# Optimization experiments

Hardware: AMD Instinct MI355X
Metric: run time of the kernel (lower is better)

Reference implementation:

```python
import jax, jax.numpy as jnp
import numpy as np

N_NODES = 50000
N_EDGES = 800000
D_IN = 96
D_HID = 256
D_OUT = 2
N_GRAPHS = 64


def _gin_conv(x, src, dst, W1, b1, W2, b2):
    # GINConv with eps=0: MLP(x + sum_{j in N(i)} x_j)
    agg = jax.ops.segment_sum(x[src], dst, num_segments=x.shape[0])
    h = x + agg
    h = jax.nn.relu(h @ W1 + b1)
    return h @ W2 + b2


def setup_inputs() -> dict:
    key = jax.random.key(0)
    ks = jax.random.split(key, 12)
    x = jax.random.normal(ks[0], (N_NODES, D_IN), dtype=jnp.float32)
    edge_index = jax.random.randint(ks[1], (2, N_EDGES), 0, N_NODES, dtype=jnp.int64)
    batch = jnp.sort(jax.random.randint(ks[2], (N_NODES,), 0, N_GRAPHS, dtype=jnp.int64))

    def lin(k, fan_in, shape):
        bound = 1.0 / np.sqrt(fan_in)
        return jax.random.uniform(k, shape, jnp.float32, -bound, bound)

    W1 = lin(ks[3], D_IN, (D_IN, D_HID)); b1 = lin(ks[4], D_IN, (D_HID,))
    W2 = lin(ks[5], D_HID, (D_HID, D_HID)); b2 = lin(ks[6], D_HID, (D_HID,))
    V1 = lin(ks[7], D_HID, (D_HID, D_HID)); c1 = lin(ks[8], D_HID, (D_HID,))
    V2 = lin(ks[9], D_HID, (D_HID, D_HID)); c2 = lin(ks[10], D_HID, (D_HID,))
    Wl = lin(ks[11], D_HID, (D_HID, D_OUT)); bl = jnp.zeros((D_OUT,), jnp.float32)
    return {"x": x, "edge_index": edge_index, "batch": batch,
            "W1": W1, "b1": b1, "W2": W2, "b2": b2,
            "V1": V1, "c1": c1, "V2": V2, "c2": c2,
            "Wl": Wl, "bl": bl}


def reference(x, edge_index, batch, W1, b1, W2, b2, V1, c1, V2, c2, Wl, bl):
    src, dst = edge_index[0], edge_index[1]
    h = jax.nn.relu(_gin_conv(x, src, dst, W1, b1, W2, b2))
    h = _gin_conv(h, src, dst, V1, c1, V2, c2)
    # global_mean_pool over batch ids
    sums = jax.ops.segment_sum(h, batch, num_segments=N_GRAPHS)
    counts = jax.ops.segment_sum(jnp.ones((h.shape[0], 1), h.dtype), batch,
                                 num_segments=N_GRAPHS)
    pooled = sums / jnp.maximum(counts, 1.0)
    # dropout p=0.1 is identity in eval mode
    return pooled @ Wl + bl
```

## Files before the change

kernel.cpp:

```cpp
#include <hip/hip_runtime.h>

#define N_NODES 50000
#define N_EDGES 800000
#define D_IN 96
#define D_HID 256
#define N_GRAPHS 64

#define SCAN_NB ((N_NODES + 255) / 256)

typedef __attribute__((ext_vector_type(8))) short bf16x8;
typedef __attribute__((ext_vector_type(4))) float f32x4;

__device__ __forceinline__ unsigned short f2bf(float f) {
    union { float f; unsigned int u; } v; v.f = f;
    unsigned int r = (v.u + 0x7FFFu + ((v.u >> 16) & 1u)) >> 16;
    return (unsigned short)r;
}
__device__ __forceinline__ float bfLo(unsigned int u) {
    union { unsigned int u; float f; } v; v.u = u << 16; return v.f;
}
__device__ __forceinline__ float bfHi(unsigned int u) {
    union { unsigned int u; float f; } v; v.u = u & 0xFFFF0000u; return v.f;
}
__device__ __forceinline__ unsigned int packbf(float a, float b) {
    return (unsigned int)f2bf(a) | ((unsigned int)f2bf(b) << 16);
}

__global__ void k_count(const int* __restrict__ dst, int* __restrict__ deg, int E) {
    int e = blockIdx.x * blockDim.x + threadIdx.x;
    if (e < E) atomicAdd(&deg[dst[e]], 1);
}

__global__ __launch_bounds__(256) void k_scan1(const int* __restrict__ deg,
                                               int* __restrict__ bsum, int n) {
    __shared__ int red[256];
    int tid = threadIdx.x;
    int i = blockIdx.x * 256 + tid;
    red[tid] = (i < n) ? deg[i] : 0;
    __syncthreads();
    for (int off = 128; off > 0; off >>= 1) {
        if (tid < off) red[tid] += red[tid + off];
        __syncthreads();
    }
    if (tid == 0) bsum[blockIdx.x] = red[0];
}

__global__ __launch_bounds__(256) void k_scan2(int* __restrict__ bsum, int nb) {
    __shared__ int s[256];
    int tid = threadIdx.x;
    int v = (tid < nb) ? bsum[tid] : 0;
    s[tid] = v;
    __syncthreads();
    for (int off = 1; off < 256; off <<= 1) {
        int t = (tid >= off) ? s[tid - off] : 0;
        __syncthreads();
        s[tid] += t;
        __syncthreads();
    }
    if (tid < nb) bsum[tid] = s[tid] - v;
}

__global__ __launch_bounds__(256) void k_scan3(const int* __restrict__ deg,
                                               const int* __restrict__ bsum,
                                               int* __restrict__ rp,
                                               int* __restrict__ wp, int n) {
    __shared__ int s[256];
    int tid = threadIdx.x;
    int i = blockIdx.x * 256 + tid;
    int v = (i < n) ? deg[i] : 0;
    s[tid] = v;
    __syncthreads();
    for (int off = 1; off < 256; off <<= 1) {
        int t = (tid >= off) ? s[tid - off] : 0;
        __syncthreads();
        s[tid] += t;
        __syncthreads();
    }
    if (i < n) {
        int excl = s[tid] - v + bsum[blockIdx.x];
        rp[i] = excl;
        wp[i] = excl;
    }
    if (blockIdx.x == 0 && tid == 0) rp[n] = N_EDGES;
}

__global__ void k_scatter(const int* __restrict__ src, const int* __restrict__ dst,
                          int* __restrict__ wp, int* __restrict__ csr, int E) {
    int e = blockIdx.x * blockDim.x + threadIdx.x;
    if (e < E) {
        int p = atomicAdd(&wp[dst[e]], 1);
        csr[p] = src[e];
    }
}

__global__ __launch_bounds__(256) void k_x2bf(const float* __restrict__ x,
                                              unsigned short* __restrict__ xb, int n4) {
    int i = blockIdx.x * 256 + threadIdx.x;
    if (i >= n4) return;
    float4 v = ((const float4*)x)[i];
    ((uint2*)xb)[i] = make_uint2(packbf(v.x, v.y), packbf(v.z, v.w));
}

#define ACCUM(acc, v)                                    \
    do {                                                 \
        acc[0] += bfLo((v).x); acc[1] += bfHi((v).x);    \
        acc[2] += bfLo((v).y); acc[3] += bfHi((v).y);    \
        acc[4] += bfLo((v).z); acc[5] += bfHi((v).z);    \
        acc[6] += bfLo((v).w); acc[7] += bfHi((v).w);    \
    } while (0)

__global__ __launch_bounds__(256) void k_agg96b(const unsigned short* __restrict__ xb,
                                                const int* __restrict__ rp,
                                                const int* __restrict__ csr,
                                                unsigned short* __restrict__ h0, int n) {
    int wid = blockIdx.x * 4 + (threadIdx.x >> 6);
    if (wid >= n) return;
    int lane = threadIdx.x & 63;
    int grp = lane / 12;
    int sub = lane % 12;
    int s = rp[wid], e = rp[wid + 1];
    const uint4* xp = (const uint4*)xb;
    float a[8] = {0.f, 0.f, 0.f, 0.f, 0.f, 0.f, 0.f, 0.f};
    float b[8] = {0.f, 0.f, 0.f, 0.f, 0.f, 0.f, 0.f, 0.f};
    if (lane < 48) {
        int j = s + grp;
        for (; j + 4 < e; j += 8) {
            int sc0 = csr[j];
            int sc1 = csr[j + 4];
            uint4 v0 = xp[(size_t)sc0 * 12 + sub];
            uint4 v1 = xp[(size_t)sc1 * 12 + sub];
            ACCUM(a, v0);
            ACCUM(b, v1);
        }
        if (j < e) {
            int sc0 = csr[j];
            uint4 v0 = xp[(size_t)sc0 * 12 + sub];
            ACCUM(a, v0);
        }
    }
#pragma unroll
    for (int i = 0; i < 8; i++) a[i] += b[i];
#pragma unroll
    for (int i = 0; i < 8; i++) a[i] += __shfl(a[i], lane + 24, 64);
#pragma unroll
    for (int i = 0; i < 8; i++) a[i] += __shfl(a[i], lane + 12, 64);
    if (lane < 12) {
        uint4 v = xp[(size_t)wid * 12 + sub];
        ACCUM(a, v);
        uint4 o;
        o.x = packbf(a[0], a[1]); o.y = packbf(a[2], a[3]);
        o.z = packbf(a[4], a[5]); o.w = packbf(a[6], a[7]);
        ((uint4*)h0)[(size_t)wid * 12 + sub] = o;
    }
}

__global__ __launch_bounds__(256) void k_agg256b(const unsigned short* __restrict__ h,
                                                 const int* __restrict__ rp,
                                                 const int* __restrict__ csr,
                                                 unsigned short* __restrict__ outb, int n) {
    int wid = blockIdx.x * 4 + (threadIdx.x >> 6);
    if (wid >= n) return;
    int lane = threadIdx.x & 63;
    int half = lane >> 5;
    int sub = lane & 31;
    int s = rp[wid], e = rp[wid + 1];
    const uint4* hp = (const uint4*)h;
    float a[8] = {0.f, 0.f, 0.f, 0.f, 0.f, 0.f, 0.f, 0.f};
    float b[8] = {0.f, 0.f, 0.f, 0.f, 0.f, 0.f, 0.f, 0.f};
    int j = s + half;
    for (; j + 2 < e; j += 4) {
        int sc0 = csr[j];
        int sc1 = csr[j + 2];
        uint4 v0 = hp[(size_t)sc0 * 32 + sub];
        uint4 v1 = hp[(size_t)sc1 * 32 + sub];
        ACCUM(a, v0);
        ACCUM(b, v1);
    }
    if (j < e) {
        int sc0 = csr[j];
        uint4 v0 = hp[(size_t)sc0 * 32 + sub];
        ACCUM(a, v0);
    }
#pragma unroll
    for (int i = 0; i < 8; i++) a[i] += b[i];
#pragma unroll
    for (int i = 0; i < 8; i++) a[i] += __shfl(a[i], sub + 32, 64);
    if (half == 0) {
        uint4 v = hp[(size_t)wid * 32 + sub];
        ACCUM(a, v);
        uint4 o;
        o.x = packbf(a[0], a[1]); o.y = packbf(a[2], a[3]);
        o.z = packbf(a[4], a[5]); o.w = packbf(a[6], a[7]);
        ((uint4*)outb)[(size_t)wid * 32 + sub] = o;
    }
}

__global__ __launch_bounds__(256) void k_wt(const float* __restrict__ W,
                                            unsigned short* __restrict__ Wt, int K) {
    int idx = blockIdx.x * 256 + threadIdx.x;
    if (idx >= K * 256) return;
    int k = idx >> 8;
    int n = idx & 255;
    Wt[(size_t)n * K + k] = f2bf(W[idx]);
}

template <int K, bool RELU, bool OUTBF>
__global__ __launch_bounds__(256) void gemm_mfma(const unsigned short* __restrict__ A,
                                                 const unsigned short* __restrict__ Wt,
                                                 const float* __restrict__ bias,
                                                 void* __restrict__ Cv, int M) {
    constexpr int BM = 64, BN = 128, BK = 64;
    __shared__ unsigned short As[BM][BK + 8];
    __shared__ unsigned short Bs[BN][BK + 8];
    const int tid = threadIdx.x;
    const int lane = tid & 63;
    const int wid = tid >> 6;
    const int wm = wid >> 1;
    const int wn = wid & 1;
    const int row0 = blockIdx.x * BM;
    const int col0 = blockIdx.y * BN;

    f32x4 acc[2][4];
#pragma unroll
    for (int f = 0; f < 2; f++)
#pragma unroll
        for (int g = 0; g < 4; g++) acc[f][g] = (f32x4){0.f, 0.f, 0.f, 0.f};

    for (int kt = 0; kt < K; kt += BK) {
        __syncthreads();
        {
            int m = tid >> 2;
            int kc = (tid & 3) * 16;
            int gr = row0 + m;
            uint4 w0 = make_uint4(0u, 0u, 0u, 0u), w1 = w0;
            int k = kt + kc;
            if (gr < M && k < K) {
                w0 = *(const uint4*)&A[(size_t)gr * K + k];
                if (k + 8 < K) w1 = *(const uint4*)&A[(size_t)gr * K + k + 8];
            }
            uint4* dst = (uint4*)&As[m][kc];
            dst[0] = w0; dst[1] = w1;
        }
        {
            int n = tid >> 1;
            int kc = (tid & 1) * 32;
            uint4 w[4];
#pragma unroll
            for (int i = 0; i < 4; i++) {
                int k = kt + kc + i * 8;
                if (k < K)
                    w[i] = *(const uint4*)&Wt[(size_t)(col0 + n) * K + k];
                else
                    w[i] = make_uint4(0u, 0u, 0u, 0u);
            }
            uint4* dst = (uint4*)&Bs[n][kc];
#pragma unroll
            for (int i = 0; i < 4; i++) dst[i] = w[i];
        }
        __syncthreads();
#pragma unroll
        for (int ks = 0; ks < 2; ks++) {
            int ko = ks * 32 + (lane >> 4) * 8;
            bf16x8 af[2], bfr[4];
#pragma unroll
            for (int f = 0; f < 2; f++)
                af[f] = *(const bf16x8*)&As[wm * 32 + f * 16 + (lane & 15)][ko];
#pragma unroll
            for (int g = 0; g < 4; g++)
                bfr[g] = *(const bf16x8*)&Bs[wn * 64 + g * 16 + (lane & 15)][ko];
#pragma unroll
            for (int f = 0; f < 2; f++)
#pragma unroll
                for (int g = 0; g < 4; g++)
                    acc[f][g] = __builtin_amdgcn_mfma_f32_16x16x32_bf16(
                        af[f], bfr[g], acc[f][g], 0, 0, 0);
        }
    }

#pragma unroll
    for (int g = 0; g < 4; g++) {
        int n = col0 + wn * 64 + g * 16 + (lane & 15);
        float bb = bias[n];
#pragma unroll
        for (int f = 0; f < 2; f++) {
#pragma unroll
            for (int r = 0; r < 4; r++) {
                int m = row0 + wm * 32 + f * 16 + (lane >> 4) * 4 + r;
                if (m < M) {
                    float v = acc[f][g][r] + bb;
                    if (RELU) v = fmaxf(v, 0.f);
                    if (OUTBF)
                        ((unsigned short*)Cv)[(size_t)m * 256 + n] = f2bf(v);
                    else
                        ((float*)Cv)[(size_t)m * 256 + n] = v;
                }
            }
        }
    }
}

#define POOL_ROWS 64
__global__ __launch_bounds__(256) void k_pool_partial(const unsigned short* __restrict__ h,
                                                      const int* __restrict__ batch,
                                                      float* __restrict__ psum, int n) {
    int r0 = blockIdx.x * POOL_ROWS;
    int r1 = r0 + POOL_ROWS;
    if (r1 > n) r1 = n;
    if (r0 >= r1) return;
    int c = threadIdx.x;
    float acc = 0.f;
    int g = batch[r0];
    for (int r = r0; r < r1; r++) {
        int gr = batch[r];
        if (gr != g) {
            atomicAdd(&psum[g * 256 + c], acc);
            acc = 0.f;
            g = gr;
        }
        acc += bfLo((unsigned int)h[(size_t)r * 256 + c]);
    }
    atomicAdd(&psum[g * 256 + c], acc);
}

__device__ __forceinline__ int lower_bound_i(const int* __restrict__ a, int n, int v) {
    int lo = 0, hi = n;
    while (lo < hi) {
        int mid = (lo + hi) >> 1;
        if (a[mid] < v) lo = mid + 1; else hi = mid;
    }
    return lo;
}

__global__ __launch_bounds__(128) void k_head(const float* __restrict__ psum,
                                              const int* __restrict__ batch,
                                              const float* __restrict__ Wl,
                                              const float* __restrict__ bl,
                                              float* __restrict__ out, int n) {
    int tid = threadIdx.x;
    int g = tid >> 1, o = tid & 1;
    int s = lower_bound_i(batch, n, g);
    int e = lower_bound_i(batch, n, g + 1);
    float inv = 1.0f / (float)((e - s) > 1 ? (e - s) : 1);
    float sum = bl[o];
    for (int k = 0; k < 256; k++)
        sum = fmaf(psum[g * 256 + k] * inv, Wl[k * 2 + o], sum);
    out[g * 2 + o] = sum;
}

extern "C" void kernel_launch(void* const* d_in, const int* in_sizes, int n_in,
                              void* d_out, int out_size, void* d_ws, size_t ws_size,
                              hipStream_t stream) {
    const float* x = (const float*)d_in[0];
    const int* ei = (const int*)d_in[1];
    const int* batch = (const int*)d_in[2];
    const float* W1 = (const float*)d_in[3];
    const float* b1 = (const float*)d_in[4];
    const float* W2 = (const float*)d_in[5];
    const float* b2 = (const float*)d_in[6];
    const float* V1 = (const float*)d_in[7];
    const float* c1 = (const float*)d_in[8];
    const float* V2 = (const float*)d_in[9];
    const float* c2 = (const float*)d_in[10];
    const float* Wl = (const float*)d_in[11];
    const float* bl = (const float*)d_in[12];
    float* out = (float*)d_out;

    const int* srcp = ei;
    const int* dstp = ei + N_EDGES;

    char* ws = (char*)d_ws;
    size_t off = 0;
    auto alloc = [&](size_t bytes) {
        size_t o = off;
        off = (off + bytes + 255) & ~(size_t)255;
        return o;
    };
    size_t o_deg = alloc(sizeof(int) * (N_NODES + 1));
    size_t o_rp = alloc(sizeof(int) * (N_NODES + 1));
    size_t o_wp = alloc(sizeof(int) * (N_NODES + 1));
    size_t o_bsum = alloc(sizeof(int) * SCAN_NB);
    size_t o_csr = alloc(sizeof(int) * N_EDGES);
    size_t o_B1 = alloc(sizeof(unsigned short) * (size_t)N_NODES * D_HID);
    size_t o_B2 = alloc(sizeof(unsigned short) * (size_t)N_NODES * D_HID);
    size_t o_pool = alloc(sizeof(float) * N_GRAPHS * D_HID);
    size_t o_wt1 = alloc(sizeof(unsigned short) * D_IN * D_HID);
    size_t o_wt2 = alloc(sizeof(unsigned short) * D_HID * D_HID);
    size_t o_wv1 = alloc(sizeof(unsigned short) * D_HID * D_HID);
    size_t o_wv2 = alloc(sizeof(unsigned short) * D_HID * D_HID);
    (void)ws_size;

    int* deg = (int*)(ws + o_deg);
    int* rp = (int*)(ws + o_rp);
    int* wp = (int*)(ws + o_wp);
    int* bsum = (int*)(ws + o_bsum);
    int* csr = (int*)(ws + o_csr);
    unsigned short* B1 = (unsigned short*)(ws + o_B1);
    unsigned short* B2 = (unsigned short*)(ws + o_B2);
    float* psum = (float*)(ws + o_pool);
    unsigned short* wt1 = (unsigned short*)(ws + o_wt1);
    unsigned short* wt2 = (unsigned short*)(ws + o_wt2);
    unsigned short* wv1 = (unsigned short*)(ws + o_wv1);
    unsigned short* wv2 = (unsigned short*)(ws + o_wv2);

    hipMemsetAsync(deg, 0, sizeof(int) * (N_NODES + 1), stream);
    hipMemsetAsync(psum, 0, sizeof(float) * N_GRAPHS * D_HID, stream);

    k_wt<<<D_IN, 256, 0, stream>>>(W1, wt1, D_IN);
    k_wt<<<D_HID, 256, 0, stream>>>(W2, wt2, D_HID);
    k_wt<<<D_HID, 256, 0, stream>>>(V1, wv1, D_HID);
    k_wt<<<D_HID, 256, 0, stream>>>(V2, wv2, D_HID);

    k_count<<<(N_EDGES + 255) / 256, 256, 0, stream>>>(dstp, deg, N_EDGES);
    k_scan1<<<SCAN_NB, 256, 0, stream>>>(deg, bsum, N_NODES);
    k_scan2<<<1, 256, 0, stream>>>(bsum, SCAN_NB);
    k_scan3<<<SCAN_NB, 256, 0, stream>>>(deg, bsum, rp, wp, N_NODES);
    k_scatter<<<(N_EDGES + 255) / 256, 256, 0, stream>>>(srcp, dstp, wp, csr, N_EDGES);

    k_x2bf<<<(N_NODES * D_IN / 4 + 255) / 256, 256, 0, stream>>>(x, B1, N_NODES * D_IN / 4);

    dim3 ggrid((N_NODES + 63) / 64, 2);

    k_agg96b<<<(N_NODES + 3) / 4, 256, 0, stream>>>(B1, rp, csr, B2, N_NODES);
    gemm_mfma<96, true, true><<<ggrid, 256, 0, stream>>>(B2, wt1, b1, B1, N_NODES);
    gemm_mfma<256, true, true><<<ggrid, 256, 0, stream>>>(B1, wt2, b2, B2, N_NODES);

    k_agg256b<<<(N_NODES + 3) / 4, 256, 0, stream>>>(B2, rp, csr, B1, N_NODES);
    gemm_mfma<256, true, true><<<ggrid, 256, 0, stream>>>(B1, wv1, c1, B2, N_NODES);
    gemm_mfma<256, false, true><<<ggrid, 256, 0, stream>>>(B2, wv2, c2, B1, N_NODES);

    k_pool_partial<<<(N_NODES + POOL_ROWS - 1) / POOL_ROWS, 256, 0, stream>>>(
        B1, batch, psum, N_NODES);
    k_head<<<1, 128, 0, stream>>>(psum, batch, Wl, bl, out, N_NODES);
}
```

Before: 338.6 us.

## Fuse each GIN layer's two GEMMs into one kernel with LDS-resident hidden tile

Replaces the pair of MFMA GEMM launches per GIN layer with a single kernel that computes the first linear+ReLU into a 64x256 bf16 tile kept in shared memory, then multiplies it by the second weight matrix. Each block now covers all 256 output columns, so the intermediate activation never goes through global memory and two launches are removed. In exchange, LDS use grows to roughly 80KB per block and the accumulators double, which can lower occupancy. The grid also shrinks to one dimension, giving half as many blocks.

```diff
diff --git a/kernel.cpp b/kernel.cpp
--- a/kernel.cpp
+++ b/kernel.cpp
@@ -204,29 +204,30 @@
     Wt[(size_t)n * K + k] = f2bf(W[idx]);
 }
 
-template <int K, bool RELU, bool OUTBF>
-__global__ __launch_bounds__(256) void gemm_mfma(const unsigned short* __restrict__ A,
-                                                 const unsigned short* __restrict__ Wt,
-                                                 const float* __restrict__ bias,
-                                                 void* __restrict__ Cv, int M) {
-    constexpr int BM = 64, BN = 128, BK = 64;
-    __shared__ unsigned short As[BM][BK + 8];
-    __shared__ unsigned short Bs[BN][BK + 8];
+template <int K1, bool RELU2>
+__global__ __launch_bounds__(256) void fused_mlp(const unsigned short* __restrict__ A,
+                                                 const unsigned short* __restrict__ W1t,
+                                                 const float* __restrict__ bias1,
+                                                 const unsigned short* __restrict__ W2t,
+                                                 const float* __restrict__ bias2,
+                                                 unsigned short* __restrict__ C, int M) {
+    __shared__ unsigned short As[64][72];
+    __shared__ unsigned short Bs[256][72];
+    __shared__ unsigned short T1[64][264];
     const int tid = threadIdx.x;
     const int lane = tid & 63;
     const int wid = tid >> 6;
     const int wm = wid >> 1;
     const int wn = wid & 1;
-    const int row0 = blockIdx.x * BM;
-    const int col0 = blockIdx.y * BN;
-
-    f32x4 acc[2][4];
+    const int row0 = blockIdx.x * 64;
+
+    f32x4 acc[2][8];
 #pragma unroll
     for (int f = 0; f < 2; f++)
 #pragma unroll
-        for (int g = 0; g < 4; g++) acc[f][g] = (f32x4){0.f, 0.f, 0.f, 0.f};
-
-    for (int kt = 0; kt < K; kt += BK) {
+        for (int g = 0; g < 8; g++) acc[f][g] = (f32x4){0.f, 0.f, 0.f, 0.f};
+
+    for (int kt = 0; kt < K1; kt += 64) {
         __syncthreads();
         {
             int m = tid >> 2;
@@ -234,24 +235,23 @@
             int gr = row0 + m;
             uint4 w0 = make_uint4(0u, 0u, 0u, 0u), w1 = w0;
             int k = kt + kc;
-            if (gr < M && k < K) {
-                w0 = *(const uint4*)&A[(size_t)gr * K + k];
-                if (k + 8 < K) w1 = *(const uint4*)&A[(size_t)gr * K + k + 8];
+            if (gr < M && k < K1) {
+                w0 = *(const uint4*)&A[(size_t)gr * K1 + k];
+                if (k + 8 < K1) w1 = *(const uint4*)&A[(size_t)gr * K1 + k + 8];
             }
             uint4* dst = (uint4*)&As[m][kc];
             dst[0] = w0; dst[1] = w1;
         }
-        {
-            int n = tid >> 1;
+#pragma unroll
+        for (int p = 0; p < 2; p++) {
+            int n = (tid >> 1) + p * 128;
             int kc = (tid & 1) * 32;
             uint4 w[4];
 #pragma unroll
             for (int i = 0; i < 4; i++) {
                 int k = kt + kc + i * 8;
-                if (k < K)
-                    w[i] = *(const uint4*)&Wt[(size_t)(col0 + n) * K + k];
-                else
-                    w[i] = make_uint4(0u, 0u, 0u, 0u);
+                w[i] = (k < K1) ? *(const uint4*)&W1t[(size_t)n * K1 + k]
+                                : make_uint4(0u, 0u, 0u, 0u);
             }
             uint4* dst = (uint4*)&Bs[n][kc];
 #pragma unroll
@@ -261,26 +261,81 @@
 #pragma unroll
         for (int ks = 0; ks < 2; ks++) {
             int ko = ks * 32 + (lane >> 4) * 8;
-            bf16x8 af[2], bfr[4];
+            bf16x8 af[2], bfr[8];
 #pragma unroll
             for (int f = 0; f < 2; f++)
                 af[f] = *(const bf16x8*)&As[wm * 32 + f * 16 + (lane & 15)][ko];
 #pragma unroll
-            for (int g = 0; g < 4; g++)
-                bfr[g] = *(const bf16x8*)&Bs[wn * 64 + g * 16 + (lane & 15)][ko];
+            for (int g = 0; g < 8; g++)
+                bfr[g] = *(const bf16x8*)&Bs[wn * 128 + g * 16 + (lane & 15)][ko];
 #pragma unroll
             for (int f = 0; f < 2; f++)
 #pragma unroll
-                for (int g = 0; g < 4; g++)
+                for (int g = 0; g < 8; g++)
                     acc[f][g] = __builtin_amdgcn_mfma_f32_16x16x32_bf16(
                         af[f], bfr[g], acc[f][g], 0, 0, 0);
         }
     }
 
 #pragma unroll
-    for (int g = 0; g < 4; g++) {
-        int n = col0 + wn * 64 + g * 16 + (lane & 15);
-        float bb = bias[n];
+    for (int g = 0; g < 8; g++) {
+        int col = wn * 128 + g * 16 + (lane & 15);
+        float bb = bias1[col];
+#pragma unroll
+        for (int f = 0; f < 2; f++) {
+#pragma unroll
+            for (int r = 0; r < 4; r++) {
+                int row = wm * 32 + f * 16 + (lane >> 4) * 4 + r;
+                float v = fmaxf(acc[f][g][r] + bb, 0.f);
+                T1[row][col] = f2bf(v);
+            }
+        }
+    }
+#pragma unroll
+    for (int f = 0; f < 2; f++)
+#pragma unroll
+        for (int g = 0; g < 8; g++) acc[f][g] = (f32x4){0.f, 0.f, 0.f, 0.f};
+
+    for (int kt = 0; kt < 256; kt += 64) {
+        __syncthreads();
+#pragma unroll
+        for (int p = 0; p < 2; p++) {
+            int n = (tid >> 1) + p * 128;
+            int kc = (tid & 1) * 32;
+            uint4 w[4];
+#pragma unroll
+            for (int i = 0; i < 4; i++) {
+                int k = kt + kc + i * 8;
+                w[i] = *(const uint4*)&W2t[(size_t)n * 256 + k];
+            }
+            uint4* dst = (uint4*)&Bs[n][kc];
+#pragma unroll
+            for (int i = 0; i < 4; i++) dst[i] = w[i];
+        }
+        __syncthreads();
+#pragma unroll
+        for (int ks = 0; ks < 2; ks++) {
+            int ko = ks * 32 + (lane >> 4) * 8;
+            bf16x8 af[2], bfr[8];
+#pragma unroll
+            for (int f = 0; f < 2; f++)
+                af[f] = *(const bf16x8*)&T1[wm * 32 + f * 16 + (lane & 15)][kt + ko];
+#pragma unroll
+            for (int g = 0; g < 8; g++)
+                bfr[g] = *(const bf16x8*)&Bs[wn * 128 + g * 16 + (lane & 15)][ko];
+#pragma unroll
+            for (int f = 0; f < 2; f++)
+#pragma unroll
+                for (int g = 0; g < 8; g++)
+                    acc[f][g] = __builtin_amdgcn_mfma_f32_16x16x32_bf16(
+                        af[f], bfr[g], acc[f][g], 0, 0, 0);
+        }
+    }
+
+#pragma unroll
+    for (int g = 0; g < 8; g++) {
+        int n = wn * 128 + g * 16 + (lane & 15);
+        float bb = bias2[n];
 #pragma unroll
         for (int f = 0; f < 2; f++) {
 #pragma unroll
@@ -288,11 +343,8 @@
                 int m = row0 + wm * 32 + f * 16 + (lane >> 4) * 4 + r;
                 if (m < M) {
                     float v = acc[f][g][r] + bb;
-                    if (RELU) v = fmaxf(v, 0.f);
-                    if (OUTBF)
-                        ((unsigned short*)Cv)[(size_t)m * 256 + n] = f2bf(v);
-                    else
-                        ((float*)Cv)[(size_t)m * 256 + n] = v;
+                    if (RELU2) v = fmaxf(v, 0.f);
+                    C[(size_t)m * 256 + n] = f2bf(v);
                 }
             }
         }
@@ -418,15 +470,13 @@
 
     k_x2bf<<<(N_NODES * D_IN / 4 + 255) / 256, 256, 0, stream>>>(x, B1, N_NODES * D_IN / 4);
 
-    dim3 ggrid((N_NODES + 63) / 64, 2);
+    int mlpgrid = (N_NODES + 63) / 64;
 
     k_agg96b<<<(N_NODES + 3) / 4, 256, 0, stream>>>(B1, rp, csr, B2, N_NODES);
-    gemm_mfma<96, true, true><<<ggrid, 256, 0, stream>>>(B2, wt1, b1, B1, N_NODES);
-    gemm_mfma<256, true, true><<<ggrid, 256, 0, stream>>>(B1, wt2, b2, B2, N_NODES);
-
-    k_agg256b<<<(N_NODES + 3) / 4, 256, 0, stream>>>(B2, rp, csr, B1, N_NODES);
-    gemm_mfma<256, true, true><<<ggrid, 256, 0, stream>>>(B1, wv1, c1, B2, N_NODES);
-    gemm_mfma<256, false, true><<<ggrid, 256, 0, stream>>>(B2, wv2, c2, B1, N_NODES);
+    fused_mlp<96, true><<<mlpgrid, 256, 0, stream>>>(B2, wt1, b1, wt2, b2, B1, N_NODES);
+
+    k_agg256b<<<(N_NODES + 3) / 4, 256, 0, stream>>>(B1, rp, csr, B2, N_NODES);
+    fused_mlp<256, false><<<mlpgrid, 256, 0, stream>>>(B2, wv1, c1, wv2, c2, B1, N_NODES);
 
     k_pool_partial<<<(N_NODES + POOL_ROWS - 1) / POOL_ROWS, 256, 0, stream>>>(
         B1, batch, psum, N_NODES);
```

Measured after the change: 333.1 us. No clear change (-1.6%).
